# Optimization experiments

Measured on AMD Instinct MI355X. Metric: run time of the kernel, lower is better.

Reference implementation:

```python
import jax, jax.numpy as jnp
import numpy as np

N_NODES = 10000
N_EDGES = 160000
D_IN = 512
D_OUT = 512
LEAKY_SLOPE = 0.01  # F.leaky_relu default negative_slope
EPS = 1e-12         # F.normalize default eps


def setup_inputs() -> dict:
    key = jax.random.key(0)
    k1, k2, k3, k4, k5, k6 = jax.random.split(key, 6)
    x = jax.random.normal(k1, (N_NODES, D_IN), dtype=jnp.float32)
    src = jax.random.randint(k2, (N_EDGES,), 0, N_NODES, dtype=jnp.int64)
    dst = jax.random.randint(k3, (N_EDGES,), 0, N_NODES, dtype=jnp.int64)
    scale = 1.0 / np.sqrt(D_IN)
    W_self = jax.random.normal(k4, (D_IN, D_OUT), dtype=jnp.float32) * scale
    W_neigh = jax.random.normal(k5, (D_IN, D_OUT), dtype=jnp.float32) * scale
    b = jax.random.normal(k6, (D_OUT,), dtype=jnp.float32) * scale
    return {"x": x, "src": src, "dst": dst, "W_self": W_self, "W_neigh": W_neigh, "b": b}


def reference(x, src, dst, W_self, W_neigh, b):
    # mean aggregation over in-neighbors: gather source features, scatter-add to dst
    msg_sum = jax.ops.segment_sum(x[src], dst, num_segments=N_NODES)  # [N, D_IN]
    deg = jax.ops.segment_sum(jnp.ones((src.shape[0],), x.dtype), dst, num_segments=N_NODES)
    neigh = msg_sum / jnp.maximum(deg, 1.0)[:, None]
    # SAGEConv: self transform + neighbor transform + bias
    h = x @ W_self + neigh @ W_neigh + b
    # leaky_relu then row-wise L2 normalize
    h = jnp.where(h >= 0, h, LEAKY_SLOPE * h)
    norm = jnp.sqrt(jnp.sum(h * h, axis=1, keepdims=True))
    return h / jnp.maximum(norm, EPS)
```

## Files before the change

kernel.cpp:

```cpp
#include <hip/hip_runtime.h>
#include <hip/hip_bf16.h>
#include <hip/hip_fp8.h>

#define N_NODES 10000
#define N_EDGES 160000
#define D_IN 512
#define D_OUT 512
#define K_TOT 1024
#define BK 64
#define SLOTS 128

typedef __attribute__((ext_vector_type(8))) short short8;
typedef __attribute__((ext_vector_type(4))) float f32x4;
typedef __attribute__((ext_vector_type(2))) float f32x2;

__device__ __forceinline__ void load_lds16(const void* g, void* l) {
    __builtin_amdgcn_global_load_lds(
        (const __attribute__((address_space(1))) void*)g,
        (__attribute__((address_space(3))) void*)l, 16, 0, 0);
}

__device__ __forceinline__ float bf16_to_f32(unsigned short u) {
    union { unsigned int i; float f; } c;
    c.i = ((unsigned int)u) << 16;
    return c.f;
}

#if defined(__has_builtin) && __has_builtin(__builtin_amdgcn_cvt_pk_fp8_f32) && \
    __has_builtin(__builtin_amdgcn_cvt_pk_f32_fp8)
#define HW_FP8 1
#else
#define HW_FP8 0
#endif

__device__ __forceinline__ unsigned int enc_fp8x4(float a, float b, float c, float d) {
#if HW_FP8
    int v = __builtin_amdgcn_cvt_pk_fp8_f32(a, b, 0, false);
    v = __builtin_amdgcn_cvt_pk_fp8_f32(c, d, v, true);
    return (unsigned int)v;
#else
    __hip_fp8_e4m3 q0(a), q1(b), q2(c), q3(d);
    return (unsigned int)q0.__x | ((unsigned int)q1.__x << 8) |
           ((unsigned int)q2.__x << 16) | ((unsigned int)q3.__x << 24);
#endif
}

__device__ __forceinline__ void dec_fp8x4_add(float* acc, unsigned int v) {
#if HW_FP8
    f32x2 lo = __builtin_amdgcn_cvt_pk_f32_fp8((int)v, false);
    f32x2 hi = __builtin_amdgcn_cvt_pk_f32_fp8((int)v, true);
    acc[0] += lo.x; acc[1] += lo.y; acc[2] += hi.x; acc[3] += hi.y;
#else
#pragma unroll
    for (int i = 0; i < 4; ++i) {
        __hip_fp8_e4m3 q; q.__x = (unsigned char)(v >> (8 * i));
        acc[i] += (float)q;
    }
#endif
}


__global__ __launch_bounds__(256) void k1_prep(const int* __restrict__ src,
                                               const int* __restrict__ dst,
                                               int* __restrict__ deg,
                                               int* __restrict__ csr_src,
                                               const float* __restrict__ Wself,
                                               const float* __restrict__ Wneigh,
                                               __hip_bfloat16* __restrict__ Wt,
                                               const float* __restrict__ x,
                                               __hip_bfloat16* __restrict__ A,
                                               unsigned int* __restrict__ x8) {
    int bid = blockIdx.x;
    int tid = threadIdx.x;
    if (bid < 625) {
        int e = bid * 256 + tid;
        int d = dst[e];
        int slot = atomicAdd(&deg[d], 1);
        if (slot < SLOTS) csr_src[d * SLOTS + slot] = src[e];
        return;
    }
    if (bid < 1137) {
        __shared__ float tl[32][33];
        int b = bid - 625;
        int kt0 = (b & 31) * 32;
        int nt0 = (b >> 5) * 32;
        int tx = tid & 31, ty = tid >> 5;
        const float* Wsrc = (kt0 < D_IN) ? (Wself + (size_t)kt0 * D_OUT)
                                         : (Wneigh + (size_t)(kt0 - D_IN) * D_OUT);
#pragma unroll
        for (int p = 0; p < 4; ++p)
            tl[p * 8 + ty][tx] = Wsrc[(size_t)(p * 8 + ty) * D_OUT + nt0 + tx];
        __syncthreads();
#pragma unroll
        for (int p = 0; p < 4; ++p)
            Wt[(size_t)(nt0 + p * 8 + ty) * K_TOT + kt0 + tx] =
                __float2bfloat16(tl[tx][p * 8 + ty]);
        return;
    }
    int gid = (bid - 1137) * 256 + tid;
    int row = gid >> 6;
    int col = (gid & 63) * 8;
    const float4* p = (const float4*)(x + (size_t)row * D_IN + col);
    float4 u = p[0], v = p[1];
    union { short8 s; __hip_bfloat16 h[8]; } o;
    o.h[0] = __float2bfloat16(u.x); o.h[1] = __float2bfloat16(u.y);
    o.h[2] = __float2bfloat16(u.z); o.h[3] = __float2bfloat16(u.w);
    o.h[4] = __float2bfloat16(v.x); o.h[5] = __float2bfloat16(v.y);
    o.h[6] = __float2bfloat16(v.z); o.h[7] = __float2bfloat16(v.w);
    *(short8*)(A + (size_t)row * K_TOT + col) = o.s;
    uint2 q;
    q.x = enc_fp8x4(u.x, u.y, u.z, u.w);
    q.y = enc_fp8x4(v.x, v.y, v.z, v.w);
    *(uint2*)(x8 + ((size_t)row * D_IN + col) / 4) = q;
}


__global__ __launch_bounds__(256) void aggregate_kernel(const int* __restrict__ deg,
                                                        const int* __restrict__ csr_src,
                                                        const unsigned int* __restrict__ x8,
                                                        __hip_bfloat16* __restrict__ A) {
    int wave = threadIdx.x >> 6, lane = threadIdx.x & 63;
    int node = blockIdx.x * 4 + wave;
    if (node >= N_NODES) return;
    int cnt = deg[node];
    if (cnt > SLOTS) cnt = SLOTS;
    const int* ebase = csr_src + (size_t)node * SLOTS;
    const int w0 = lane * 2;
    float acc[8];
#pragma unroll
    for (int i = 0; i < 8; ++i) acc[i] = 0.f;
    for (int base = 0; base < cnt; base += 64) {
        int m = cnt - base; if (m > 64) m = 64;
        int idx = (base + lane < cnt) ? ebase[base + lane] : 0;
        int j = 0;
        for (; j + 3 < m; j += 4) {
            int s0 = __shfl(idx, j), s1 = __shfl(idx, j + 1);
            int s2 = __shfl(idx, j + 2), s3 = __shfl(idx, j + 3);
            uint2 v0 = *(const uint2*)(x8 + (size_t)s0 * (D_IN / 4) + w0);
            uint2 v1 = *(const uint2*)(x8 + (size_t)s1 * (D_IN / 4) + w0);
            uint2 v2 = *(const uint2*)(x8 + (size_t)s2 * (D_IN / 4) + w0);
            uint2 v3 = *(const uint2*)(x8 + (size_t)s3 * (D_IN / 4) + w0);
            dec_fp8x4_add(acc, v0.x); dec_fp8x4_add(acc + 4, v0.y);
            dec_fp8x4_add(acc, v1.x); dec_fp8x4_add(acc + 4, v1.y);
            dec_fp8x4_add(acc, v2.x); dec_fp8x4_add(acc + 4, v2.y);
            dec_fp8x4_add(acc, v3.x); dec_fp8x4_add(acc + 4, v3.y);
        }
        for (; j < m; ++j) {
            int s0 = __shfl(idx, j);
            uint2 v0 = *(const uint2*)(x8 + (size_t)s0 * (D_IN / 4) + w0);
            dec_fp8x4_add(acc, v0.x); dec_fp8x4_add(acc + 4, v0.y);
        }
    }
    float inv = 1.0f / fmaxf((float)cnt, 1.0f);
    union { short8 s; __hip_bfloat16 h[8]; } o;
#pragma unroll
    for (int i = 0; i < 8; ++i) o.h[i] = __float2bfloat16(acc[i] * inv);
    *(short8*)(A + (size_t)node * K_TOT + D_IN + lane * 8) = o.s;
}


__global__ __launch_bounds__(256, 3) void gemm_kernel(const short* __restrict__ A,
                                                      const short* __restrict__ Wt,
                                                      const float* __restrict__ bias,
                                                      float* __restrict__ H) {
    __shared__ __align__(16) short smA[2][128 * BK];
    __shared__ __align__(16) short smB[2][64 * BK];
    const int tid = threadIdx.x;
    const int wave = tid >> 6, lane = tid & 63;

    const int s = (blockIdx.x & 7) * 79 + (blockIdx.x >> 3);
    const int m0 = (s >> 3) * 128;
    const int n0 = (s & 7) * 64;

    const int wm = wave >> 1, wn = wave & 1;
    const int rr = lane & 15, kq = lane >> 4;

    const int srow8 = lane >> 3;
    const int sslot = (lane & 7) ^ srow8;

    f32x4 acc[4][2];
#pragma unroll
    for (int i = 0; i < 4; ++i)
#pragma unroll
        for (int j = 0; j < 2; ++j) acc[i][j] = (f32x4){0.f, 0.f, 0.f, 0.f};

    int garow[4];
#pragma unroll
    for (int i = 0; i < 4; ++i) {
        int gr = m0 + (wave + 4 * i) * 8 + srow8;
        garow[i] = (gr > N_NODES - 1) ? N_NODES - 1 : gr;
    }
    int gbrow[2];
#pragma unroll
    for (int i = 0; i < 2; ++i) gbrow[i] = n0 + (wave + 4 * i) * 8 + srow8;

    auto stage = [&](int buf, int kt) {
        const int kbase = kt * BK + sslot * 8;
#pragma unroll
        for (int i = 0; i < 4; ++i)
            load_lds16(A + (size_t)garow[i] * K_TOT + kbase,
                       (char*)smA[buf] + (wave + 4 * i) * 1024);
#pragma unroll
        for (int i = 0; i < 2; ++i)
            load_lds16(Wt + (size_t)gbrow[i] * K_TOT + kbase,
                       (char*)smB[buf] + (wave + 4 * i) * 1024);
    };

    stage(0, 0);
    __syncthreads();

    for (int kt = 0; kt < K_TOT / BK; ++kt) {
        const int cur = kt & 1;
        if (kt + 1 < K_TOT / BK) stage(cur ^ 1, kt + 1);

        short8 afr[2][4], bfr[2][2];
#pragma unroll
        for (int ks = 0; ks < 2; ++ks) {
#pragma unroll
            for (int mf = 0; mf < 4; ++mf) {
                int row = wm * 64 + mf * 16 + rr;
                int slot = (ks * 4 + kq) ^ (row & 7);
                afr[ks][mf] = *(const short8*)&smA[cur][row * 64 + slot * 8];
            }
#pragma unroll
            for (int nf = 0; nf < 2; ++nf) {
                int row = wn * 32 + nf * 16 + rr;
                int slot = (ks * 4 + kq) ^ (row & 7);
                bfr[ks][nf] = *(const short8*)&smB[cur][row * 64 + slot * 8];
            }
        }
#pragma unroll
        for (int ks = 0; ks < 2; ++ks)
#pragma unroll
            for (int mf = 0; mf < 4; ++mf)
#pragma unroll
                for (int nf = 0; nf < 2; ++nf)
                    acc[mf][nf] = __builtin_amdgcn_mfma_f32_16x16x32_bf16(
                        afr[ks][mf], bfr[ks][nf], acc[mf][nf], 0, 0, 0);
        __syncthreads();
    }

#pragma unroll
    for (int mf = 0; mf < 4; ++mf) {
        int row = m0 + wm * 64 + mf * 16 + kq * 4;
#pragma unroll
        for (int nf = 0; nf < 2; ++nf) {
            int col = n0 + wn * 32 + nf * 16 + rr;
            float bv = bias[col];
#pragma unroll
            for (int r = 0; r < 4; ++r) {
                int grow = row + r;
                if (grow < N_NODES) {
                    float v = acc[mf][nf][r] + bv;
                    v = (v >= 0.f) ? v : 0.01f * v;
                    H[(size_t)grow * D_OUT + col] = v;
                }
            }
        }
    }
}


__global__ __launch_bounds__(256) void normalize_kernel(float* __restrict__ H) {
    int wave = threadIdx.x >> 6, lane = threadIdx.x & 63;
    int row = blockIdx.x * 4 + wave;
    if (row >= N_NODES) return;
    float4* p = (float4*)(H + (size_t)row * D_OUT + lane * 8);
    float4 u = p[0], v = p[1];
    float s = u.x * u.x + u.y * u.y + u.z * u.z + u.w * u.w +
              v.x * v.x + v.y * v.y + v.z * v.z + v.w * v.w;
#pragma unroll
    for (int o = 32; o > 0; o >>= 1) s += __shfl_xor(s, o);
    float scale = 1.0f / fmaxf(sqrtf(s), 1e-12f);
    u.x *= scale; u.y *= scale; u.z *= scale; u.w *= scale;
    v.x *= scale; v.y *= scale; v.z *= scale; v.w *= scale;
    p[0] = u; p[1] = v;
}


extern "C" void kernel_launch(void* const* d_in, const int* in_sizes, int n_in,
                              void* d_out, int out_size, void* d_ws, size_t ws_size,
                              hipStream_t stream) {
    const float* x      = (const float*)d_in[0];
    const int*   src    = (const int*)d_in[1];
    const int*   dst    = (const int*)d_in[2];
    const float* Wself  = (const float*)d_in[3];
    const float* Wneigh = (const float*)d_in[4];
    const float* bias   = (const float*)d_in[5];
    float* H = (float*)d_out;

    char* ws = (char*)d_ws;
    int* deg     = (int*)ws;
    int* csr_src = deg + N_NODES;
    size_t int_bytes = ((size_t)(N_NODES + N_NODES * SLOTS) * 4 + 255) & ~(size_t)255;
    __hip_bfloat16* Abuf = (__hip_bfloat16*)(ws + int_bytes);
    __hip_bfloat16* Wt   = Abuf + (size_t)N_NODES * K_TOT;
    unsigned int*   x8   = (unsigned int*)(Wt + (size_t)D_OUT * K_TOT);

    hipMemsetAsync(deg, 0, N_NODES * sizeof(int), stream);

    k1_prep<<<625 + 512 + 2500, 256, 0, stream>>>(src, dst, deg, csr_src,
                                                  Wself, Wneigh, Wt, x, Abuf, x8);
    aggregate_kernel<<<2500, 256, 0, stream>>>(deg, csr_src, x8, Abuf);
    gemm_kernel<<<632, 256, 0, stream>>>((const short*)Abuf, (const short*)Wt, bias, H);
    normalize_kernel<<<2500, 256, 0, stream>>>(H);
}
```

Measured before the change: 68.29 us.

## Use 128x128 GEMM tiles with BK=32 and XCD-aware block remap

Widens the GEMM output tile from 128x64 to 128x128, so each wave computes a 64x64 sub-tile with 16 MFMAs per k-step. The k-step shrinks to 32 and the LDS swizzle changes to match. The block count halves to 316 and uses a new XCD-grouped work-id mapping. The aim is more reuse of A and B per LDS load and less redundant A traffic, at the cost of more accumulator registers, fewer blocks on 256 CUs, and twice as many k-iterations and barriers.

New measurement: 75.61 us. +10.7%, slower.

```diff
diff --git a/kernel.cpp b/kernel.cpp
--- a/kernel.cpp
+++ b/kernel.cpp
@@ -7,7 +7,6 @@
 #define D_IN 512
 #define D_OUT 512
 #define K_TOT 1024
-#define BK 64
 #define SLOTS 128
 
 typedef __attribute__((ext_vector_type(8))) short short8;
@@ -163,80 +162,78 @@
                                                       const short* __restrict__ Wt,
                                                       const float* __restrict__ bias,
                                                       float* __restrict__ H) {
-    __shared__ __align__(16) short smA[2][128 * BK];
-    __shared__ __align__(16) short smB[2][64 * BK];
+    __shared__ __align__(16) short smA[2][128 * 32];
+    __shared__ __align__(16) short smB[2][128 * 32];
     const int tid = threadIdx.x;
     const int wave = tid >> 6, lane = tid & 63;
 
-    const int s = (blockIdx.x & 7) * 79 + (blockIdx.x >> 3);
-    const int m0 = (s >> 3) * 128;
-    const int n0 = (s & 7) * 64;
+    const int xcd = blockIdx.x & 7;
+    const int k = blockIdx.x >> 3;
+    const int wgid = ((xcd < 4) ? xcd * 40 : 160 + (xcd - 4) * 39) + k;
+    const int m0 = (wgid >> 2) * 128;
+    const int n0 = (wgid & 3) * 128;
 
     const int wm = wave >> 1, wn = wave & 1;
     const int rr = lane & 15, kq = lane >> 4;
-
-    const int srow8 = lane >> 3;
-    const int sslot = (lane & 7) ^ srow8;
-
-    f32x4 acc[4][2];
+    const int grr = (rr & 3) ^ ((rr >> 2) & 3);
+
+    const int lrow = lane >> 2;
+    const int schunk = (lane & 3) ^ ((lane >> 2) & 3) ^ ((lane >> 4) & 3);
+
+    f32x4 acc[4][4];
 #pragma unroll
     for (int i = 0; i < 4; ++i)
 #pragma unroll
-        for (int j = 0; j < 2; ++j) acc[i][j] = (f32x4){0.f, 0.f, 0.f, 0.f};
-
-    int garow[4];
-#pragma unroll
-    for (int i = 0; i < 4; ++i) {
-        int gr = m0 + (wave + 4 * i) * 8 + srow8;
+        for (int j = 0; j < 4; ++j) acc[i][j] = (f32x4){0.f, 0.f, 0.f, 0.f};
+
+    int garow[2];
+#pragma unroll
+    for (int i = 0; i < 2; ++i) {
+        int gr = m0 + wave * 32 + i * 16 + lrow;
         garow[i] = (gr > N_NODES - 1) ? N_NODES - 1 : gr;
     }
     int gbrow[2];
 #pragma unroll
-    for (int i = 0; i < 2; ++i) gbrow[i] = n0 + (wave + 4 * i) * 8 + srow8;
+    for (int i = 0; i < 2; ++i) gbrow[i] = n0 + wave * 32 + i * 16 + lrow;
 
     auto stage = [&](int buf, int kt) {
-        const int kbase = kt * BK + sslot * 8;
-#pragma unroll
-        for (int i = 0; i < 4; ++i)
-            load_lds16(A + (size_t)garow[i] * K_TOT + kbase,
-                       (char*)smA[buf] + (wave + 4 * i) * 1024);
+        const int kb = kt * 32 + schunk * 8;
 #pragma unroll
         for (int i = 0; i < 2; ++i)
-            load_lds16(Wt + (size_t)gbrow[i] * K_TOT + kbase,
-                       (char*)smB[buf] + (wave + 4 * i) * 1024);
+            load_lds16(A + (size_t)garow[i] * K_TOT + kb,
+                       (char*)smA[buf] + (wave * 32 + i * 16) * 64);
+#pragma unroll
+        for (int i = 0; i < 2; ++i)
+            load_lds16(Wt + (size_t)gbrow[i] * K_TOT + kb,
+                       (char*)smB[buf] + (wave * 32 + i * 16) * 64);
     };
 
     stage(0, 0);
     __syncthreads();
 
-    for (int kt = 0; kt < K_TOT / BK; ++kt) {
+    for (int kt = 0; kt < K_TOT / 32; ++kt) {
         const int cur = kt & 1;
-        if (kt + 1 < K_TOT / BK) stage(cur ^ 1, kt + 1);
-
-        short8 afr[2][4], bfr[2][2];
-#pragma unroll
-        for (int ks = 0; ks < 2; ++ks) {
-#pragma unroll
-            for (int mf = 0; mf < 4; ++mf) {
-                int row = wm * 64 + mf * 16 + rr;
-                int slot = (ks * 4 + kq) ^ (row & 7);
-                afr[ks][mf] = *(const short8*)&smA[cur][row * 64 + slot * 8];
-            }
-#pragma unroll
-            for (int nf = 0; nf < 2; ++nf) {
-                int row = wn * 32 + nf * 16 + rr;
-                int slot = (ks * 4 + kq) ^ (row & 7);
-                bfr[ks][nf] = *(const short8*)&smB[cur][row * 64 + slot * 8];
-            }
-        }
-#pragma unroll
-        for (int ks = 0; ks < 2; ++ks)
-#pragma unroll
-            for (int mf = 0; mf < 4; ++mf)
-#pragma unroll
-                for (int nf = 0; nf < 2; ++nf)
-                    acc[mf][nf] = __builtin_amdgcn_mfma_f32_16x16x32_bf16(
-                        afr[ks][mf], bfr[ks][nf], acc[mf][nf], 0, 0, 0);
+        if (kt + 1 < K_TOT / 32) stage(cur ^ 1, kt + 1);
+
+        short8 afr[4], bfr[4];
+#pragma unroll
+        for (int mf = 0; mf < 4; ++mf) {
+            int row = wm * 64 + mf * 16 + rr;
+            int pch = kq ^ grr;
+            afr[mf] = *(const short8*)&smA[cur][row * 32 + pch * 8];
+        }
+#pragma unroll
+        for (int nf = 0; nf < 4; ++nf) {
+            int row = wn * 64 + nf * 16 + rr;
+            int pch = kq ^ grr;
+            bfr[nf] = *(const short8*)&smB[cur][row * 32 + pch * 8];
+        }
+#pragma unroll
+        for (int mf = 0; mf < 4; ++mf)
+#pragma unroll
+            for (int nf = 0; nf < 4; ++nf)
+                acc[mf][nf] = __builtin_amdgcn_mfma_f32_16x16x32_bf16(
+                    afr[mf], bfr[nf], acc[mf][nf], 0, 0, 0);
         __syncthreads();
     }
 
@@ -244,8 +241,8 @@
     for (int mf = 0; mf < 4; ++mf) {
         int row = m0 + wm * 64 + mf * 16 + kq * 4;
 #pragma unroll
-        for (int nf = 0; nf < 2; ++nf) {
-            int col = n0 + wn * 32 + nf * 16 + rr;
+        for (int nf = 0; nf < 4; ++nf) {
+            int col = n0 + wn * 64 + nf * 16 + rr;
             float bv = bias[col];
 #pragma unroll
             for (int r = 0; r < 4; ++r) {
@@ -302,6 +299,6 @@
     k1_prep<<<625 + 512 + 2500, 256, 0, stream>>>(src, dst, deg, csr_src,
                                                   Wself, Wneigh, Wt, x, Abuf, x8);
     aggregate_kernel<<<2500, 256, 0, stream>>>(deg, csr_src, x8, Abuf);
-    gemm_kernel<<<632, 256, 0, stream>>>((const short*)Abuf, (const short*)Wt, bias, H);
+    gemm_kernel<<<316, 256, 0, stream>>>((const short*)Abuf, (const short*)Wt, bias, H);
     normalize_kernel<<<2500, 256, 0, stream>>>(H);
 }
```
